# Optimization experiments

Hardware: AMD Instinct MI355X
Metric: run time of the kernel (lower is better)

The kernel has to match this reference:

```python
import jax, jax.numpy as jnp
import numpy as np

B, T, I, F, M, O = 256, 512, 128, 512, 512, 128


def setup_inputs() -> dict:
    key = jax.random.key(0)
    ks = jax.random.split(key, 12)
    def lin(k, out_d, in_d):
        std = 1.0 / np.sqrt(in_d)
        kw, kb = jax.random.split(k)
        W = jax.random.uniform(kw, (out_d, in_d), jnp.float32, -std, std)
        b = jax.random.uniform(kb, (out_d,), jnp.float32, -std, std)
        return W, b
    Wi2f, bi2f = lin(ks[0], F, I)
    Wm2f, bm2f = lin(ks[1], F, M)
    Wf2m, bf2m = lin(ks[2], M, F)
    Wm2m, bm2m = lin(ks[3], M, M)
    Wout, bout = lin(ks[4], O, M)
    x = jax.random.normal(ks[5], (B, T, I), jnp.float32)
    m0 = jnp.zeros((B, M), jnp.float32)
    return {"x": x, "m0": m0,
            "Wi2f": Wi2f, "bi2f": bi2f, "Wm2f": Wm2f, "bm2f": bm2f,
            "Wf2m": Wf2m, "bf2m": bf2m, "Wm2m": Wm2m, "bm2m": bm2m,
            "Wout": Wout, "bout": bout}


def reference(x, m0, Wi2f, bi2f, Wm2f, bm2f, Wf2m, bf2m, Wm2m, bm2m, Wout, bout):
    # Precompute input->functional projection for all timesteps (batched GEMM).
    xp = jnp.einsum('bti,fi->btf', x, Wi2f) + bi2f  # (B, T, F)

    def step(m, xp_t):
        f = jnp.tanh(xp_t + m @ Wm2f.T + bm2f)           # (B, F)
        m_new = (f @ Wf2m.T + bf2m) + (m @ Wm2m.T + bm2m)  # (B, M)
        return m_new, m_new

    m_last, _ms = jax.lax.scan(step, m0, jnp.swapaxes(xp, 0, 1))  # ms: (T, B, M)
    # OUTPUT_TYPE.LAST_OUT: output layer applied to final memory state.
    return m_last @ Wout.T + bout  # (B, O)
```

## Files before the change

kernel.cpp:

```cpp
#include <hip/hip_runtime.h>
#include <hip/hip_bf16.h>

typedef __bf16 bf16x8 __attribute__((ext_vector_type(8)));
typedef __bf16 bf16x4 __attribute__((ext_vector_type(4)));
typedef float  f32x4  __attribute__((ext_vector_type(4)));
typedef unsigned int u32;
typedef unsigned long long u64;

static __device__ __forceinline__ void mfma_z(f32x4& d, bf16x8 a, const f32x4& b) {
    asm("v_mfma_f32_16x16x32_bf16 %0, %1, %2, 0"
        : "=&v"(d) : "v"(a), "a"(b));
}
static __device__ __forceinline__ void mfma_a(f32x4& d, bf16x8 a, const f32x4& b) {
    asm("v_mfma_f32_16x16x32_bf16 %0, %1, %2, %0"
        : "+v"(d) : "v"(a), "a"(b));
}
#define ACC_GUARD(e, o) asm volatile("s_nop 7\n\ts_nop 7" : "+v"(e), "+v"(o))

static __device__ __forceinline__ f32x4 mfma16(bf16x8 a, bf16x8 b, f32x4 c) {
    return __builtin_amdgcn_mfma_f32_16x16x32_bf16(a, b, c, 0, 0, 0);
}

static __device__ __forceinline__ void poll_flags(const u32* flags, u32 tgt,
                                                  int lane, u32& alive) {
    if (!alive) return;
    for (u32 it = 0; it < (1u << 22); ++it) {
        u32 v = __hip_atomic_load(&flags[lane & 7], __ATOMIC_RELAXED, __HIP_MEMORY_SCOPE_AGENT);
        if (__all((int)(v >= tgt))) return;
    }
    alive = 0;
}

#define TLEN 512
#define IDIM 128
#define FDIM 512
#define MDIM 512
#define ODIM 128
#define BC   8
#define NGRP 32
#define NCU  8
#define PSTR 520
#define XSTR 136
#define SSTR 24

#define WS_WI   0
#define WS_W2F  (WS_WI  + FDIM*IDIM*2)
#define WS_W2M  (WS_W2F + FDIM*MDIM*2)
#define WS_WF2  (WS_W2M + MDIM*MDIM*2)
#define WS_WO   (WS_WF2 + MDIM*FDIM*2)
#define WS_C    (WS_WO  + ODIM*MDIM*2)
#define WS_D    (WS_C   + FDIM*FDIM*2)
#define WS_B1   (WS_D   + MDIM*FDIM*2)
#define WS_B23  (WS_B1  + FDIM*4)
#define WS_CB   (WS_B23 + MDIM*4)
#define WS_CU   (WS_CB  + FDIM*4)
#define WS_FLG  (WS_CU  + MDIM*4)
#define WS_BUF  (WS_FLG + NGRP*64*4)

#define N_WI  (FDIM*IDIM)
#define N_W2F (FDIM*MDIM)
#define N_W2M (MDIM*MDIM)
#define N_WF2 (MDIM*FDIM)
#define N_WO  (ODIM*MDIM)

__global__ __launch_bounds__(256) void lmn_prep1(
    const float* __restrict__ Wi2f, const float* __restrict__ Wm2f,
    const float* __restrict__ Wm2m, const float* __restrict__ Wf2m,
    const float* __restrict__ Wout,
    const float* __restrict__ bi2f, const float* __restrict__ bm2f,
    const float* __restrict__ bf2m, const float* __restrict__ bm2m,
    __bf16* __restrict__ WI, __bf16* __restrict__ W2F, __bf16* __restrict__ W2M,
    __bf16* __restrict__ WF2, __bf16* __restrict__ WO,
    float* __restrict__ b1, float* __restrict__ b23, u32* __restrict__ flags)
{
    int i = blockIdx.x * 256 + threadIdx.x;
    if (i < N_WI)  { WI[i]  = (__bf16)Wi2f[i]; return; }  i -= N_WI;
    if (i < N_W2F) { W2F[i] = (__bf16)Wm2f[i]; return; }  i -= N_W2F;
    if (i < N_W2M) { W2M[i] = (__bf16)Wm2m[i]; return; }  i -= N_W2M;
    if (i < N_WF2) { WF2[i] = (__bf16)Wf2m[i]; return; }  i -= N_WF2;
    if (i < N_WO)  { WO[i]  = (__bf16)Wout[i]; return; }  i -= N_WO;
    if (i < FDIM)  { b1[i]  = bi2f[i] + bm2f[i]; return; } i -= FDIM;
    if (i < MDIM)  { b23[i] = bf2m[i] + bm2m[i]; return; } i -= MDIM;
    if (i < NGRP * 64) { flags[i] = 0u; return; }
}

__global__ __launch_bounds__(256) void lmn_prep2(
    const float* __restrict__ Wm2f, const float* __restrict__ Wm2m,
    const float* __restrict__ Wf2m,
    const float* __restrict__ b1, const float* __restrict__ b23,
    __bf16* __restrict__ C, __bf16* __restrict__ D,
    float* __restrict__ cb, float* __restrict__ cu)
{
    int bb = blockIdx.x;
    if (bb < 2048) {
        int row = bb >> 1;
        int k   = (bb & 1) * 256 + threadIdx.x;
        const float* A = (row < 512) ? Wm2f : Wm2m;
        int r = row & 511;
        float acc = 0.f;
        for (int j = 0; j < 512; ++j)
            acc += A[(size_t)r * 512 + j] * Wf2m[(size_t)j * 512 + k];
        if (row < 512) C[(size_t)r * 512 + k] = (__bf16)acc;
        else           D[(size_t)r * 512 + k] = (__bf16)acc;
        return;
    }
    int idx = (bb - 2048) * 256 + threadIdx.x;
    if (idx < 512) {
        float acc = b1[idx];
        for (int j = 0; j < 512; ++j) acc += Wm2f[(size_t)idx * 512 + j] * b23[j];
        cb[idx] = acc;
    } else {
        int r = idx - 512;
        float acc = 0.f;
        for (int j = 0; j < 512; ++j) acc += Wm2m[(size_t)r * 512 + j] * b23[j];
        cu[r] = acc;
    }
}

__global__ __launch_bounds__(512, 2) void lmn_scan(
    const float* __restrict__ x, const float* __restrict__ m0,
    const __bf16* __restrict__ WI, const __bf16* __restrict__ W2F,
    const __bf16* __restrict__ W2M, const __bf16* __restrict__ Cm,
    const __bf16* __restrict__ Dm, const __bf16* __restrict__ WF2,
    const __bf16* __restrict__ WO,
    const float* __restrict__ b1, const float* __restrict__ cb,
    const float* __restrict__ cu, const float* __restrict__ b23,
    const float* __restrict__ bout,
    u32* __restrict__ flags_all, __bf16* __restrict__ buf,
    float* __restrict__ out)
{
    __shared__ __bf16 ulds[BC][PSTR];
    __shared__ __bf16 flds[BC][PSTR];
    __shared__ __bf16 xlds[BC][XSTR];
    __shared__ __bf16 sstg[8][BC][SSTR];

    const int tid  = threadIdx.x;
    const int lane = tid & 63;
    const int w    = tid >> 6;
    const int wq   = w & 3;
    const int l15  = lane & 15;
    const int l4   = lane >> 4;
    const int koff = 8 * l4;
    const int ar   = l15 & 7;
    const bool sRole = (w < 4);

    const int b = blockIdx.x;
    const int g = b & 31;
    const int p = b >> 5;
    const int row0 = g * BC;

    u32* flags = flags_all + g * 64;
    u32  alive = 1;

    const int c0 = 64 * p + 16 * wq + l15;

    f32x4 wgt[36];
    {
        const __bf16* rA = (sRole ? W2F : W2M) + (size_t)c0 * MDIM;
        const __bf16* rC = (sRole ? Cm  : Dm ) + (size_t)c0 * FDIM;
        #pragma unroll
        for (int j = 0; j < 16; ++j) {
            int kk = (2 * p + j) & 15;
            wgt[j]      = *(const f32x4*)&rA[kk * 32 + koff];
            wgt[16 + j] = *(const f32x4*)&rC[kk * 32 + koff];
        }
        if (sRole) {
            const __bf16* rX = WI + (size_t)c0 * IDIM;
            #pragma unroll
            for (int j = 0; j < 4; ++j) wgt[32 + j] = *(const f32x4*)&rX[j * 32 + koff];
        } else {
            #pragma unroll
            for (int j = 32; j < 36; ++j) wgt[j] = f32x4{0, 0, 0, 0};
        }
        #pragma unroll
        for (int j = 0; j < 36; ++j) asm volatile("" : "+a"(wgt[j]));
    }
    const float b1r = sRole ? b1[c0] : 0.f;
    const float cbr = sRole ? cb[c0] : 0.f;
    const float cur = sRole ? 0.f    : cu[c0];

    {
        int row = tid >> 6, col8 = (tid & 63) << 3;
        const float* ms = &m0[(size_t)(row0 + row) * MDIM + col8];
        float4 v0 = ((const float4*)ms)[0], v1 = ((const float4*)ms)[1];
        *(bf16x8*)&ulds[row][col8] =
            bf16x8{(__bf16)v0.x, (__bf16)v0.y, (__bf16)v0.z, (__bf16)v0.w,
                   (__bf16)v1.x, (__bf16)v1.y, (__bf16)v1.z, (__bf16)v1.w};
    }
    if (tid < 128) {
        int rr = tid >> 4, c8 = (tid & 15) << 3;
        const float* xs = &x[(size_t)(row0 + rr) * TLEN * IDIM + c8];
        float4 v0 = ((const float4*)xs)[0], v1 = ((const float4*)xs)[1];
        *(bf16x8*)&xlds[rr][c8] =
            bf16x8{(__bf16)v0.x, (__bf16)v0.y, (__bf16)v0.z, (__bf16)v0.w,
                   (__bf16)v1.x, (__bf16)v1.y, (__bf16)v1.z, (__bf16)v1.w};
    }
    __syncthreads();

    f32x4 accE, accO;
    {
        bf16x8 a0 = *(const bf16x8*)&ulds[ar][((2 * p + 0) & 15) * 32 + koff];
        bf16x8 a1 = *(const bf16x8*)&ulds[ar][((2 * p + 1) & 15) * 32 + koff];
        mfma_z(accE, a0, wgt[0]);  mfma_z(accO, a1, wgt[1]);
        #pragma unroll
        for (int j = 2; j < 16; ++j) {
            bf16x8 am = *(const bf16x8*)&ulds[ar][((2 * p + j) & 15) * 32 + koff];
            if (j & 1) mfma_a(accO, am, wgt[j]);
            else       mfma_a(accE, am, wgt[j]);
        }
        if (sRole) {
            #pragma unroll
            for (int j = 0; j < 4; ++j) {
                bf16x8 ax = *(const bf16x8*)&xlds[ar][j * 32 + koff];
                if (j & 1) mfma_a(accO, ax, wgt[32 + j]);
                else       mfma_a(accE, ax, wgt[32 + j]);
            }
        }
    }

    for (int t = 0; t < TLEN; ++t) {
        ACC_GUARD(accE, accO);
        f32x4 va = accE + accO;
        if (l4 < 2) {
            if (sRole) {
                const float addc = (t == 0) ? b1r : cbr;
                #pragma unroll
                for (int r = 0; r < 4; ++r)
                    sstg[w][4 * l4 + r][l15] = (__bf16)tanhf(va[r] + addc);
            } else {
                const float addu = (t == 0) ? 0.f : cur;
                #pragma unroll
                for (int r = 0; r < 4; ++r)
                    sstg[w][4 * l4 + r][l15] = (__bf16)(va[r] + addu);
            }
        }
        asm volatile("s_waitcnt lgkmcnt(0)" ::: "memory");

        const size_t bufbase = (size_t)((t & 1) * NGRP + g) * (2 * BC * MDIM);
        if (lane < 32) {
            const int mat  = sRole ? 1 : 0;
            const int erow = lane & 7, eq = lane >> 3;
            u64 v = *(const u64*)&sstg[w][erow][4 * eq];
            __bf16* dst = buf + bufbase + (size_t)mat * (BC * MDIM)
                        + erow * MDIM + 64 * p + 16 * wq + 4 * eq;
            __hip_atomic_store((u64*)dst, v, __ATOMIC_RELAXED, __HIP_MEMORY_SCOPE_AGENT);
        }
        asm volatile("s_waitcnt vmcnt(0)" ::: "memory");
        __syncthreads();
        if (tid == 0)
            __hip_atomic_store(&flags[p], (u32)t + 1u,
                               __ATOMIC_RELAXED, __HIP_MEMORY_SCOPE_AGENT);

        if (t + 1 < TLEN) {
            const int cc = 8 * (l4 & 1);
            bf16x8 au0 = *(const bf16x8*)&sstg[4 + (l4 >> 1)][ar][cc];
            bf16x8 au1 = *(const bf16x8*)&sstg[6 + (l4 >> 1)][ar][cc];
            bf16x8 af0 = *(const bf16x8*)&sstg[0 + (l4 >> 1)][ar][cc];
            bf16x8 af1 = *(const bf16x8*)&sstg[2 + (l4 >> 1)][ar][cc];
            mfma_z(accE, au0, wgt[0]);   mfma_z(accO, au1, wgt[1]);
            mfma_a(accE, af0, wgt[16]);  mfma_a(accO, af1, wgt[17]);
        }

        if (tid < 128 && t + 1 < TLEN) {
            int rr = tid >> 4, c8 = (tid & 15) << 3;
            const float* xs = &x[((size_t)(row0 + rr) * TLEN + (t + 1)) * IDIM + c8];
            float4 v0 = ((const float4*)xs)[0], v1 = ((const float4*)xs)[1];
            *(bf16x8*)&xlds[rr][c8] =
                bf16x8{(__bf16)v0.x, (__bf16)v0.y, (__bf16)v0.z, (__bf16)v0.w,
                       (__bf16)v1.x, (__bf16)v1.y, (__bf16)v1.z, (__bf16)v1.w};
        }
        poll_flags(flags, (u32)t + 1u, lane, alive);

        {
            int mat = tid >> 8, rem = tid & 255;
            int row = rem >> 5, col16 = (rem & 31) << 4;
            const __bf16* src = buf + bufbase + (size_t)mat * (BC * MDIM)
                              + row * MDIM + col16;
            u64 q0 = __hip_atomic_load((const u64*)src,     __ATOMIC_RELAXED, __HIP_MEMORY_SCOPE_AGENT);
            u64 q1 = __hip_atomic_load((const u64*)src + 1, __ATOMIC_RELAXED, __HIP_MEMORY_SCOPE_AGENT);
            u64 q2 = __hip_atomic_load((const u64*)src + 2, __ATOMIC_RELAXED, __HIP_MEMORY_SCOPE_AGENT);
            u64 q3 = __hip_atomic_load((const u64*)src + 3, __ATOMIC_RELAXED, __HIP_MEMORY_SCOPE_AGENT);
            __bf16* dl = mat ? &flds[row][col16] : &ulds[row][col16];
            ((u64*)dl)[0] = q0; ((u64*)dl)[1] = q1;
            ((u64*)dl)[2] = q2; ((u64*)dl)[3] = q3;
        }
        __syncthreads();

        if (t == TLEN - 1) break;

        {
            #pragma unroll
            for (int j = 2; j < 16; ++j) {
                bf16x8 am = *(const bf16x8*)&ulds[ar][((2 * p + j) & 15) * 32 + koff];
                if (j & 1) mfma_a(accO, am, wgt[j]);
                else       mfma_a(accE, am, wgt[j]);
            }
            #pragma unroll
            for (int j = 2; j < 16; ++j) {
                bf16x8 af = *(const bf16x8*)&flds[ar][((2 * p + j) & 15) * 32 + koff];
                if (j & 1) mfma_a(accO, af, wgt[16 + j]);
                else       mfma_a(accE, af, wgt[16 + j]);
            }
            if (sRole) {
                #pragma unroll
                for (int j = 0; j < 4; ++j) {
                    bf16x8 ax = *(const bf16x8*)&xlds[ar][j * 32 + koff];
                    if (j & 1) mfma_a(accO, ax, wgt[32 + j]);
                    else       mfma_a(accE, ax, wgt[32 + j]);
                }
            }
        }
    }

    if (p == 0) {
        f32x4 ma[4];
        #pragma unroll
        for (int nt = 0; nt < 4; ++nt) {
            int ct = 64 * w + 16 * nt + l15;
            f32x4 acc = {0, 0, 0, 0};
            #pragma unroll
            for (int j = 0; j < 16; ++j) {
                bf16x8 af = *(const bf16x8*)&flds[ar][j * 32 + koff];
                bf16x8 bw = *(const bf16x8*)&WF2[(size_t)ct * FDIM + j * 32 + koff];
                acc = mfma16(af, bw, acc);
            }
            ma[nt] = acc;
        }
        #pragma unroll
        for (int nt = 0; nt < 4; ++nt) {
            int ct = 64 * w + 16 * nt + l15;
            if (l4 < 2) {
                #pragma unroll
                for (int r = 0; r < 4; ++r) {
                    int rr = 4 * l4 + r;
                    float mv = ma[nt][r] + (float)ulds[rr][ct] + b23[ct];
                    ulds[rr][ct] = (__bf16)mv;
                }
            }
        }
        __syncthreads();
        const int oc = 16 * w + l15;
        const __bf16* ro = WO + (size_t)oc * MDIM;
        f32x4 oe = {0, 0, 0, 0}, oo = {0, 0, 0, 0};
        #pragma unroll
        for (int j = 0; j < 16; ++j) {
            bf16x8 am = *(const bf16x8*)&ulds[ar][j * 32 + koff];
            bf16x8 bw = *(const bf16x8*)&ro[j * 32 + koff];
            if (j & 1) oo = mfma16(am, bw, oo); else oe = mfma16(am, bw, oe);
        }
        f32x4 oa = oe + oo;
        const float bo = bout[oc];
        if (l4 < 2) {
            #pragma unroll
            for (int r = 0; r < 4; ++r) {
                int rr = 4 * l4 + r;
                out[(size_t)(row0 + rr) * ODIM + oc] = oa[r] + bo;
            }
        }
    }
}

extern "C" void kernel_launch(void* const* d_in, const int* in_sizes, int n_in,
                              void* d_out, int out_size, void* d_ws, size_t ws_size,
                              hipStream_t stream)
{
    const float* x    = (const float*)d_in[0];
    const float* m0   = (const float*)d_in[1];
    const float* Wi2f = (const float*)d_in[2];
    const float* bi2f = (const float*)d_in[3];
    const float* Wm2f = (const float*)d_in[4];
    const float* bm2f = (const float*)d_in[5];
    const float* Wf2m = (const float*)d_in[6];
    const float* bf2m = (const float*)d_in[7];
    const float* Wm2m = (const float*)d_in[8];
    const float* bm2m = (const float*)d_in[9];
    const float* Wout = (const float*)d_in[10];
    const float* bout = (const float*)d_in[11];

    char* ws = (char*)d_ws;
    __bf16* WI  = (__bf16*)(ws + WS_WI);
    __bf16* W2F = (__bf16*)(ws + WS_W2F);
    __bf16* W2M = (__bf16*)(ws + WS_W2M);
    __bf16* WF2 = (__bf16*)(ws + WS_WF2);
    __bf16* WO  = (__bf16*)(ws + WS_WO);
    __bf16* Cm  = (__bf16*)(ws + WS_C);
    __bf16* Dm  = (__bf16*)(ws + WS_D);
    float*  b1  = (float*)(ws + WS_B1);
    float*  b23 = (float*)(ws + WS_B23);
    float*  cb  = (float*)(ws + WS_CB);
    float*  cu  = (float*)(ws + WS_CU);
    u32*    flg = (u32*)(ws + WS_FLG);
    __bf16* buf = (__bf16*)(ws + WS_BUF);

    const int prep1_total = N_WI + N_W2F + N_W2M + N_WF2 + N_WO
                          + FDIM + MDIM + NGRP * 64;
    lmn_prep1<<<(prep1_total + 255) / 256, 256, 0, stream>>>(
        Wi2f, Wm2f, Wm2m, Wf2m, Wout, bi2f, bm2f, bf2m, bm2m,
        WI, W2F, W2M, WF2, WO, b1, b23, flg);

    lmn_prep2<<<2052, 256, 0, stream>>>(Wm2f, Wm2m, Wf2m, b1, b23, Cm, Dm, cb, cu);

    lmn_scan<<<NGRP * NCU, 512, 0, stream>>>(
        x, m0, WI, W2F, W2M, Cm, Dm, WF2, WO,
        b1, cb, cu, b23, bout, flg, buf, (float*)d_out);
}
```

Before: 1.537 ms.

## Double-buffer x tile and split u/f exchange into staged barriers overlapping MFMA

Makes the x staging buffer double-buffered and prefetches x two steps ahead, so the x-projection MFMAs can run before the cross-block poll instead of after. The exchange load from global is split: the u half is written to LDS and consumed by MFMAs behind a lightweight s_barrier while the f half is still being stored. All 512 threads now share the global loads evenly (two u64 per matrix each). This aims to shorten the serial critical path of each recurrent step, at the cost of an extra barrier and more live registers.

```diff
diff --git a/kernel.cpp b/kernel.cpp
--- a/kernel.cpp
+++ b/kernel.cpp
@@ -131,7 +131,7 @@
 {
     __shared__ __bf16 ulds[BC][PSTR];
     __shared__ __bf16 flds[BC][PSTR];
-    __shared__ __bf16 xlds[BC][XSTR];
+    __shared__ __bf16 xlds[2][BC][XSTR];
     __shared__ __bf16 sstg[8][BC][SSTR];
 
     const int tid  = threadIdx.x;
@@ -187,11 +187,12 @@
             bf16x8{(__bf16)v0.x, (__bf16)v0.y, (__bf16)v0.z, (__bf16)v0.w,
                    (__bf16)v1.x, (__bf16)v1.y, (__bf16)v1.z, (__bf16)v1.w};
     }
-    if (tid < 128) {
-        int rr = tid >> 4, c8 = (tid & 15) << 3;
-        const float* xs = &x[(size_t)(row0 + rr) * TLEN * IDIM + c8];
+    if (tid < 256) {
+        int xb = tid >> 7;
+        int rr = (tid >> 4) & 7, c8 = (tid & 15) << 3;
+        const float* xs = &x[((size_t)(row0 + rr) * TLEN + xb) * IDIM + c8];
         float4 v0 = ((const float4*)xs)[0], v1 = ((const float4*)xs)[1];
-        *(bf16x8*)&xlds[rr][c8] =
+        *(bf16x8*)&xlds[xb][rr][c8] =
             bf16x8{(__bf16)v0.x, (__bf16)v0.y, (__bf16)v0.z, (__bf16)v0.w,
                    (__bf16)v1.x, (__bf16)v1.y, (__bf16)v1.z, (__bf16)v1.w};
     }
@@ -211,12 +212,16 @@
         if (sRole) {
             #pragma unroll
             for (int j = 0; j < 4; ++j) {
-                bf16x8 ax = *(const bf16x8*)&xlds[ar][j * 32 + koff];
+                bf16x8 ax = *(const bf16x8*)&xlds[0][ar][j * 32 + koff];
                 if (j & 1) mfma_a(accO, ax, wgt[32 + j]);
                 else       mfma_a(accE, ax, wgt[32 + j]);
             }
         }
     }
+
+    const int grow = tid >> 6;
+    const int gcol = (tid & 63) << 3;
+    const int xc2  = (tid & 63) << 1;
 
     for (int t = 0; t < TLEN; ++t) {
         ACC_GUARD(accE, accO);
@@ -259,56 +264,58 @@
             bf16x8 af1 = *(const bf16x8*)&sstg[2 + (l4 >> 1)][ar][cc];
             mfma_z(accE, au0, wgt[0]);   mfma_z(accO, au1, wgt[1]);
             mfma_a(accE, af0, wgt[16]);  mfma_a(accO, af1, wgt[17]);
-        }
-
-        if (tid < 128 && t + 1 < TLEN) {
-            int rr = tid >> 4, c8 = (tid & 15) << 3;
-            const float* xs = &x[((size_t)(row0 + rr) * TLEN + (t + 1)) * IDIM + c8];
-            float4 v0 = ((const float4*)xs)[0], v1 = ((const float4*)xs)[1];
-            *(bf16x8*)&xlds[rr][c8] =
-                bf16x8{(__bf16)v0.x, (__bf16)v0.y, (__bf16)v0.z, (__bf16)v0.w,
-                       (__bf16)v1.x, (__bf16)v1.y, (__bf16)v1.z, (__bf16)v1.w};
-        }
+            if (sRole) {
+                const __bf16 (*xc)[XSTR] = xlds[(t + 1) & 1];
+                #pragma unroll
+                for (int j = 0; j < 4; ++j) {
+                    bf16x8 ax = *(const bf16x8*)&xc[ar][j * 32 + koff];
+                    if (j & 1) mfma_a(accO, ax, wgt[32 + j]);
+                    else       mfma_a(accE, ax, wgt[32 + j]);
+                }
+            }
+        }
+
         poll_flags(flags, (u32)t + 1u, lane, alive);
-
-        {
-            int mat = tid >> 8, rem = tid & 255;
-            int row = rem >> 5, col16 = (rem & 31) << 4;
-            const __bf16* src = buf + bufbase + (size_t)mat * (BC * MDIM)
-                              + row * MDIM + col16;
-            u64 q0 = __hip_atomic_load((const u64*)src,     __ATOMIC_RELAXED, __HIP_MEMORY_SCOPE_AGENT);
-            u64 q1 = __hip_atomic_load((const u64*)src + 1, __ATOMIC_RELAXED, __HIP_MEMORY_SCOPE_AGENT);
-            u64 q2 = __hip_atomic_load((const u64*)src + 2, __ATOMIC_RELAXED, __HIP_MEMORY_SCOPE_AGENT);
-            u64 q3 = __hip_atomic_load((const u64*)src + 3, __ATOMIC_RELAXED, __HIP_MEMORY_SCOPE_AGENT);
-            __bf16* dl = mat ? &flds[row][col16] : &ulds[row][col16];
-            ((u64*)dl)[0] = q0; ((u64*)dl)[1] = q1;
-            ((u64*)dl)[2] = q2; ((u64*)dl)[3] = q3;
-        }
-        __syncthreads();
-
-        if (t == TLEN - 1) break;
-
-        {
+        asm volatile("" ::: "memory");
+
+        const __bf16* usrc = buf + bufbase + grow * MDIM + gcol;
+        const __bf16* fsrc = usrc + (size_t)(BC * MDIM);
+        u64 uq0 = __hip_atomic_load((const u64*)usrc,     __ATOMIC_RELAXED, __HIP_MEMORY_SCOPE_AGENT);
+        u64 uq1 = __hip_atomic_load((const u64*)usrc + 1, __ATOMIC_RELAXED, __HIP_MEMORY_SCOPE_AGENT);
+        u64 fq0 = __hip_atomic_load((const u64*)fsrc,     __ATOMIC_RELAXED, __HIP_MEMORY_SCOPE_AGENT);
+        u64 fq1 = __hip_atomic_load((const u64*)fsrc + 1, __ATOMIC_RELAXED, __HIP_MEMORY_SCOPE_AGENT);
+        float2 xv = {0.f, 0.f};
+        if (t + 2 < TLEN)
+            xv = *(const float2*)&x[((size_t)(row0 + grow) * TLEN + (t + 2)) * IDIM + xc2];
+
+        { u64* dl = (u64*)&ulds[grow][gcol]; dl[0] = uq0; dl[1] = uq1; }
+        asm volatile("s_waitcnt lgkmcnt(0)" ::: "memory");
+        __builtin_amdgcn_s_barrier();
+        if (t + 1 < TLEN) {
             #pragma unroll
             for (int j = 2; j < 16; ++j) {
                 bf16x8 am = *(const bf16x8*)&ulds[ar][((2 * p + j) & 15) * 32 + koff];
                 if (j & 1) mfma_a(accO, am, wgt[j]);
                 else       mfma_a(accE, am, wgt[j]);
             }
+        }
+
+        { u64* dl = (u64*)&flds[grow][gcol]; dl[0] = fq0; dl[1] = fq1; }
+        asm volatile("s_waitcnt lgkmcnt(0)" ::: "memory");
+        __builtin_amdgcn_s_barrier();
+        if (t == TLEN - 1) break;
+        {
             #pragma unroll
             for (int j = 2; j < 16; ++j) {
                 bf16x8 af = *(const bf16x8*)&flds[ar][((2 * p + j) & 15) * 32 + koff];
                 if (j & 1) mfma_a(accO, af, wgt[16 + j]);
                 else       mfma_a(accE, af, wgt[16 + j]);
             }
-            if (sRole) {
-                #pragma unroll
-                for (int j = 0; j < 4; ++j) {
-                    bf16x8 ax = *(const bf16x8*)&xlds[ar][j * 32 + koff];
-                    if (j & 1) mfma_a(accO, ax, wgt[32 + j]);
-                    else       mfma_a(accE, ax, wgt[32 + j]);
-                }
-            }
+        }
+
+        if (t + 2 < TLEN) {
+            xlds[t & 1][grow][xc2]     = (__bf16)xv.x;
+            xlds[t & 1][grow][xc2 + 1] = (__bf16)xv.y;
         }
     }
 
```

Measured after the change: 1.548 ms. Within noise of the previous version (+0.7%).
